# Optimization experiments

Measured on AMD Instinct MI355X. Metric: run time of the kernel, lower is better.

Reference implementation:

```python
import jax, jax.numpy as jnp
import numpy as np

B, L, N, T, D, V, C = 128, 512, 1023, 511, 256, 50000, 511
EPS = 1e-6


def circular_correlation(a, b):
    # c_k = sum_i a_i * b_{(i+k) mod d}  == irfft(conj(rfft(a)) * rfft(b))
    d = a.shape[-1]
    c = jnp.fft.irfft(jnp.conj(jnp.fft.rfft(a, axis=-1)) * jnp.fft.rfft(b, axis=-1), n=d, axis=-1)
    return c / (jnp.linalg.norm(c, axis=-1, keepdims=True) + EPS)


def setup_inputs() -> dict:
    key = jax.random.key(0)
    k1, k2, k3, k4, k5, k6, k7, k8 = jax.random.split(key, 8)
    num_node = jnp.full((B,), N, dtype=jnp.int64 if jax.config.jax_enable_x64 else jnp.int32)
    # leaf slot index: leaves occupy node slots 0..L-1 (deterministic, no scatter collisions)
    slot = jnp.broadcast_to(jnp.arange(L, dtype=jnp.int32)[None, :], (B, L))
    vocab_id = jax.random.randint(k1, (B, L), 0, V, dtype=jnp.int32)
    leaf_content_id = jnp.stack([slot, vocab_id], axis=-1)  # [B, L, 2]
    content_mask = (jax.random.uniform(k2, (B, L)) < 0.9).astype(jnp.int32)
    ctype = jax.random.randint(k3, (B, T), 0, 3, dtype=jnp.int32)          # 0 = no-op, 1, 2 children
    parent = jax.random.randint(k4, (B, T), L, N, dtype=jnp.int32)         # internal node slots
    lchild = jax.random.randint(k5, (B, T), 0, N, dtype=jnp.int32)
    rchild = jax.random.randint(k6, (B, T), 0, N, dtype=jnp.int32)
    composition_info = jnp.stack([ctype, parent, lchild, rchild], axis=-1)  # [B, T, 4]
    emb_weight = jax.random.normal(k7, (V, D), dtype=jnp.float32) * 0.1
    lin_weight = jax.random.normal(k8, (C, D), dtype=jnp.float32) * 0.05
    lin_bias = jnp.zeros((C,), dtype=jnp.float32)
    return {"num_node": num_node, "leaf_content_id": leaf_content_id,
            "content_mask": content_mask, "composition_info": composition_info,
            "emb_weight": emb_weight, "lin_weight": lin_weight, "lin_bias": lin_bias}


def embed_leaf_nodes(leaf_content_id, content_mask, emb_weight):
    leaf_vec = emb_weight[leaf_content_id[:, :, 1]]          # [B, L, D]
    node_idx = leaf_content_id[:, :, 0]                      # [B, L]
    mask = content_mask != 0
    safe_idx = jnp.where(mask, node_idx, N)                  # N is out-of-bounds -> dropped
    vec = jnp.zeros((B, N, D), dtype=leaf_vec.dtype)
    vec = vec.at[jnp.arange(B)[:, None], safe_idx].set(leaf_vec, mode="drop")
    norm = jnp.linalg.norm(vec, axis=2, keepdims=True) + EPS
    return vec / norm


def compose(vec, composition_info):
    bidx = jnp.arange(B)

    def step(v, info):  # info: [B, 4] for one tree level
        t, p, l, r = info[:, 0], info[:, 1], info[:, 2], info[:, 3]
        safe_p = jnp.where(t > 0, p, 0)
        lv = v[bidx, l]                                      # [B, D]
        rv = v[bidx, r]
        two = circular_correlation(lv, rv)
        cur = v[bidx, safe_p]
        val = jnp.where((t == 1)[:, None], lv,
                        jnp.where((t == 2)[:, None], two, cur))
        return v.at[bidx, safe_p].set(val), None

    vec, _ = jax.lax.scan(step, vec, jnp.swapaxes(composition_info, 0, 1))
    return vec


def reference(num_node, leaf_content_id, content_mask, composition_info,
              emb_weight, lin_weight, lin_bias):
    vec = embed_leaf_nodes(leaf_content_id, content_mask, emb_weight)
    vec = compose(vec, composition_info)
    out = jnp.einsum("bnd,cd->bnc", vec, lin_weight) + lin_bias
    return out
```

## Files before the change

kernel.cpp:

```cpp
#include <hip/hip_runtime.h>

#define NB 128
#define NL 512
#define NN 1023
#define NT 511
#define ND 256
#define NC 511
#define EPSF 1e-6f

#define SRC_ZERO (-1)
#define SLOTC 4096
#define STEPC 8192

typedef __attribute__((ext_vector_type(8))) short short8;
typedef __attribute__((ext_vector_type(4))) float f32x4;

__device__ __forceinline__ unsigned short f2bf(float f) {
  unsigned u = __builtin_bit_cast(unsigned, f);
  u += 0x7FFFu + ((u >> 16) & 1u);
  return (unsigned short)(u >> 16);
}

__global__ void __launch_bounds__(256) embed_scatter(
    const int* __restrict__ lcid, const int* __restrict__ cmask,
    const float* __restrict__ emb, float* __restrict__ leafbuf,
    unsigned short* __restrict__ vecb) {
  int rid  = blockIdx.x * 4 + (threadIdx.x >> 6);
  int lane = threadIdx.x & 63;
  int slot = lcid[2 * rid];
  int vid  = lcid[2 * rid + 1];
  int msk  = cmask[rid];
  int b    = rid >> 9;
  float4 v = {0.f, 0.f, 0.f, 0.f};
  if (msk) v = ((const float4*)(emb + (size_t)vid * ND))[lane];
  float ss = v.x * v.x + v.y * v.y + v.z * v.z + v.w * v.w;
#pragma unroll
  for (int off = 32; off > 0; off >>= 1) ss += __shfl_down(ss, off, 64);
  ss = __shfl(ss, 0, 64);
  float inv = 1.0f / (sqrtf(ss) + EPSF);
  float4 o;
  o.x = v.x * inv; o.y = v.y * inv; o.z = v.z * inv; o.w = v.w * inv;
  ((float4*)(leafbuf + ((size_t)b * 512 + slot) * ND))[lane] = o;
  uint2 pk;
  pk.x = (unsigned)f2bf(o.x) | ((unsigned)f2bf(o.y) << 16);
  pk.y = (unsigned)f2bf(o.z) | ((unsigned)f2bf(o.w) << 16);
  ((uint2*)(vecb + ((size_t)b * NN + slot) * ND))[lane] = pk;
}

__global__ void __launch_bounds__(1024) compose_kernel(
    const int* __restrict__ info, const int* __restrict__ lcid,
    const int* __restrict__ cmask, const float* __restrict__ leafbuf,
    float* __restrict__ outbuf, int* __restrict__ fsrcG) {
  const int b    = blockIdx.x;
  const int tid  = threadIdx.x;
  const int lane = tid & 63;
  const int wav  = tid >> 6;

  __shared__ int4 sinfo4[NT];
  __shared__ int lwl[NT], lwr[NT], fwr[NT];
  __shared__ int ptr_[NT];
  __shared__ int lsA[NT], rsA[NT];
  __shared__ int lvl[NT], fsrc[NT];
  __shared__ int schedS[NT], schedL[NT], schedR[NT];
  __shared__ int offs[512], cnt[512], cnt2[512];
  __shared__ unsigned char deadF[NT], liveF[NT], lzero[512];
  __shared__ float a_st[16][256], b_st[16][512];
  __shared__ int changed, smax;

  const float* lb = leafbuf + (size_t)b * 512 * ND;
  float*       ob = outbuf + (size_t)b * NT * ND;

  const int4* ib4 = (const int4*)(info + (size_t)b * NT * 4);
  for (int i = tid; i < NT; i += 1024) sinfo4[i] = ib4[i];
  if (tid < 512) lzero[tid] = 1;
  if (tid == 0) smax = 0;
  __syncthreads();
  if (tid < NL) {
    int row = lcid[((size_t)b * NL + tid) * 2];
    lzero[row] = (cmask[(size_t)b * NL + tid] == 0) ? 1 : 0;
  }
  __syncthreads();

  const int t = tid;
  int4 m1 = {0, 0, 0, 0};
  if (t < NT) m1 = sinfo4[t];
  int l1 = -1, r1 = -1, f1 = -1;
  const int prow = 512 + t;
  for (int tp = 0; tp < NT; ++tp) {
    int4 wi = sinfo4[tp];
    if (wi.x > 0) {
      if (t < NT && tp < t) { if (wi.y == m1.z) l1 = tp; if (wi.y == m1.w) r1 = tp; }
      if (wi.y == prow) f1 = tp;
    }
  }
  if (t < NT) { lwl[t] = l1; lwr[t] = r1; fwr[t] = f1; }
  __syncthreads();

  if (t < NT) {
    int v;
    if (m1.x == 2) v = SLOTC + t;
    else if (m1.x == 1) {
      if (m1.z < 512) v = m1.z;
      else v = (l1 >= 0) ? (STEPC + l1) : SRC_ZERO;
    } else v = SRC_ZERO;
    ptr_[t] = v;
  }
  __syncthreads();
  for (int it = 0; it < 10; ++it) {
    int v = 0;
    if (t < NT) { v = ptr_[t]; if (v >= STEPC) v = ptr_[v - STEPC]; }
    __syncthreads();
    if (t < NT) ptr_[t] = v;
    __syncthreads();
  }

  auto normv = [&](int v) -> int {
    if (v >= 0 && v < 512 && lzero[v]) return SRC_ZERO;
    return v;
  };
  auto collapseW = [&](int wstep) -> int {
    int v = (sinfo4[wstep].x == 2) ? (SLOTC + wstep) : ptr_[wstep];
    return normv(v);
  };
  if (t < NT) {
    if (m1.x == 2) {
      int a = (m1.z < 512) ? normv(m1.z) : ((l1 >= 0) ? collapseW(l1) : SRC_ZERO);
      int c = (m1.w < 512) ? normv(m1.w) : ((r1 >= 0) ? collapseW(r1) : SRC_ZERO);
      lsA[t] = a; rsA[t] = c;
      deadF[t] = (a == SRC_ZERO || c == SRC_ZERO) ? 1 : 0;
    } else {
      deadF[t] = 0;
    }
    liveF[t] = 0;
    fsrc[t] = (f1 >= 0) ? collapseW(f1) : SRC_ZERO;
  }
  __syncthreads();

  for (int rounds = 0; rounds < NT; ++rounds) {
    if (tid == 0) changed = 0;
    __syncthreads();
    if (t < NT && m1.x == 2 && !deadF[t]) {
      int a = lsA[t], c = rsA[t];
      if (a >= SLOTC && deadF[a - SLOTC]) { a = SRC_ZERO; lsA[t] = a; }
      if (c >= SLOTC && deadF[c - SLOTC]) { c = SRC_ZERO; rsA[t] = c; }
      if (a == SRC_ZERO || c == SRC_ZERO) { deadF[t] = 1; changed = 1; }
    }
    __syncthreads();
    if (!changed) break;
    __syncthreads();
  }

  if (t < NT) {
    int f = fsrc[t];
    if (f >= SLOTC && deadF[f - SLOTC]) { f = SRC_ZERO; fsrc[t] = f; }
    if (f >= SLOTC) liveF[f - SLOTC] = 1;
  }
  __syncthreads();
  for (int rounds = 0; rounds < NT; ++rounds) {
    if (tid == 0) changed = 0;
    __syncthreads();
    if (t < NT && m1.x == 2 && liveF[t] && !deadF[t]) {
      int a = lsA[t], c = rsA[t];
      if (a >= SLOTC && !liveF[a - SLOTC]) { liveF[a - SLOTC] = 1; changed = 1; }
      if (c >= SLOTC && !liveF[c - SLOTC]) { liveF[c - SLOTC] = 1; changed = 1; }
    }
    __syncthreads();
    if (!changed) break;
    __syncthreads();
  }

  const bool isLive = (t < NT && m1.x == 2 && liveF[t] && !deadF[t]);

  if (t < NT) lvl[t] = 0;
  __syncthreads();
  for (int rounds = 0; rounds < NT; ++rounds) {
    if (tid == 0) changed = 0;
    __syncthreads();
    if (isLive) {
      int nl = 1, a = lsA[t], c = rsA[t];
      if (a >= SLOTC) { int dl = lvl[a - SLOTC] + 1; if (dl > nl) nl = dl; }
      if (c >= SLOTC) { int dl = lvl[c - SLOTC] + 1; if (dl > nl) nl = dl; }
      if (nl > lvl[t]) { lvl[t] = nl; changed = 1; }
    }
    __syncthreads();
    if (!changed) break;
    __syncthreads();
  }
  if (isLive) atomicMax(&smax, lvl[t]);

  if (tid < 512) { cnt[tid] = 0; cnt2[tid] = 0; }
  __syncthreads();
  if (isLive) atomicAdd(&cnt[lvl[t]], 1);
  __syncthreads();
  if (tid < 512) offs[tid] = cnt[tid];
  __syncthreads();
  for (int k = 1; k < 512; k <<= 1) {
    int v = 0;
    if (tid < 512) { v = offs[tid]; if (tid >= k) v += offs[tid - k]; }
    __syncthreads();
    if (tid < 512) offs[tid] = v;
    __syncthreads();
  }
  if (isLive) {
    int d = lvl[t];
    int pos = offs[d - 1] + atomicAdd(&cnt2[d], 1);
    schedS[pos] = t; schedL[pos] = lsA[t]; schedR[pos] = rsA[t];
  }
  __syncthreads();

  const int maxd = smax;
  for (int d = 1; d <= maxd; ++d) {
    const int base = offs[d - 1];
    const int nops = cnt[d];
    const int nch  = (nops + 15) >> 4;
    for (int ch = 0; ch < nch; ++ch) {
      int rel = ch * 16 + wav;
      if (rel < nops) {
        int my = base + rel;
        int tt = schedS[my], ls = schedL[my], rs = schedR[my];
        const float* pa = (ls < 512) ? lb + (size_t)ls * ND
                                     : ob + (size_t)(ls - SLOTC) * ND;
        const float* pb = (rs < 512) ? lb + (size_t)rs * ND
                                     : ob + (size_t)(rs - SLOTC) * ND;
        float4 av = ((const float4*)pa)[lane];
        float4 bv = ((const float4*)pb)[lane];
        ((float4*)a_st[wav])[lane] = av;
        ((float4*)b_st[wav])[lane]      = bv;
        ((float4*)b_st[wav])[lane + 64] = bv;
        const float4* a4 = (const float4*)a_st[wav];
        const float4* b4 = (const float4*)b_st[wav];
        float c0 = 0.f, c1 = 0.f, c2 = 0.f, c3 = 0.f;
        float4 B0 = b4[lane];
#pragma unroll 8
        for (int i = 0; i < 64; ++i) {
          float4 A  = a4[i];
          float4 B1 = b4[lane + i + 1];
          c0 += A.x * B0.x + A.y * B0.y + A.z * B0.z + A.w * B0.w;
          c1 += A.x * B0.y + A.y * B0.z + A.z * B0.w + A.w * B1.x;
          c2 += A.x * B0.z + A.y * B0.w + A.z * B1.x + A.w * B1.y;
          c3 += A.x * B0.w + A.y * B1.x + A.z * B1.y + A.w * B1.z;
          B0 = B1;
        }
        float ss = c0 * c0 + c1 * c1 + c2 * c2 + c3 * c3;
#pragma unroll
        for (int off = 32; off > 0; off >>= 1) ss += __shfl_down(ss, off, 64);
        ss = __shfl(ss, 0, 64);
        float inv = 1.f / (sqrtf(ss) + EPSF);
        float4 res;
        res.x = c0 * inv; res.y = c1 * inv; res.z = c2 * inv; res.w = c3 * inv;
        ((float4*)(ob + (size_t)tt * ND))[lane] = res;
      }
    }
    __syncthreads();
  }

  for (int i = tid; i < NT; i += 1024) fsrcG[b * NT + i] = fsrc[i];
}

__global__ void __launch_bounds__(256) gather_rows(
    const int* __restrict__ fsrcG, const float* __restrict__ leafbuf,
    const float* __restrict__ outbuf, unsigned short* __restrict__ vecb) {
  int rid  = blockIdx.x * 4 + (threadIdx.x >> 6);
  int lane = threadIdx.x & 63;
  int b    = rid / NT;
  int idx  = rid - b * NT;
  int s    = fsrcG[rid];
  float4 v = {0.f, 0.f, 0.f, 0.f};
  if (s >= 0) {
    const float* src = (s < 512)
        ? (leafbuf + ((size_t)b * 512 + s) * ND)
        : (outbuf + ((size_t)b * NT + (s - SLOTC)) * ND);
    v = ((const float4*)src)[lane];
  }
  uint2 pk;
  pk.x = (unsigned)f2bf(v.x) | ((unsigned)f2bf(v.y) << 16);
  pk.y = (unsigned)f2bf(v.z) | ((unsigned)f2bf(v.w) << 16);
  ((uint2*)(vecb + ((size_t)b * NN + 512 + idx) * ND))[lane] = pk;
}

__global__ void __launch_bounds__(256) cvt_w(
    const float* __restrict__ src, unsigned short* __restrict__ o) {
  int i   = blockIdx.x * 256 + threadIdx.x;
  int row = (i * 8) >> 8;
  uint4 r = {0u, 0u, 0u, 0u};
  if (row < NC) {
    const float4* v4 = (const float4*)src;
    float4 x = v4[2 * i], y = v4[2 * i + 1];
    r.x = (unsigned)f2bf(x.x) | ((unsigned)f2bf(x.y) << 16);
    r.y = (unsigned)f2bf(x.z) | ((unsigned)f2bf(x.w) << 16);
    r.z = (unsigned)f2bf(y.x) | ((unsigned)f2bf(y.y) << 16);
    r.w = (unsigned)f2bf(y.z) | ((unsigned)f2bf(y.w) << 16);
  }
  ((uint4*)o)[i] = r;
}

__global__ void __launch_bounds__(256) gemm_kernel(
    const short* __restrict__ A, const short* __restrict__ W,
    const float* __restrict__ bias, float* __restrict__ out) {
  __shared__ short As[128 * 64];
  __shared__ short Ws[128 * 64];
  int tid  = threadIdx.x;
  int lane = tid & 63;
  int w    = tid >> 6;
  int c0   = blockIdx.x * 128;
  int m0   = blockIdx.y * 128;
  int wm   = (w & 1) * 64;
  int wc   = (w >> 1) * 64;
  int frow = lane & 15;
  int quad = lane >> 4;
  f32x4 acc[4][4];
#pragma unroll
  for (int i = 0; i < 4; ++i)
#pragma unroll
    for (int j = 0; j < 4; ++j) acc[i][j] = (f32x4){0.f, 0.f, 0.f, 0.f};

  for (int k0 = 0; k0 < ND; k0 += 64) {
#pragma unroll
    for (int i = 0; i < 4; ++i) {
      int idx = i * 256 + tid;
      int row = idx >> 3;
      int ch  = idx & 7;
      const short* ga = A + (size_t)(m0 + row) * ND + k0 + ch * 8;
      const short* gw = W + (size_t)(c0 + row) * ND + k0 + ch * 8;
      __builtin_amdgcn_global_load_lds(
          (const __attribute__((address_space(1))) void*)ga,
          (__attribute__((address_space(3))) void*)(As + idx * 8), 16, 0, 0);
      __builtin_amdgcn_global_load_lds(
          (const __attribute__((address_space(1))) void*)gw,
          (__attribute__((address_space(3))) void*)(Ws + idx * 8), 16, 0, 0);
    }
    __syncthreads();
#pragma unroll
    for (int ks = 0; ks < 2; ++ks) {
      short8 af[4], wf[4];
#pragma unroll
      for (int mi = 0; mi < 4; ++mi)
        af[mi] = *(const short8*)(As + (wm + mi * 16 + frow) * 64 + ks * 32 + quad * 8);
#pragma unroll
      for (int ci = 0; ci < 4; ++ci)
        wf[ci] = *(const short8*)(Ws + (wc + ci * 16 + frow) * 64 + ks * 32 + quad * 8);
#pragma unroll
      for (int mi = 0; mi < 4; ++mi)
#pragma unroll
        for (int ci = 0; ci < 4; ++ci)
          acc[mi][ci] = __builtin_amdgcn_mfma_f32_16x16x32_bf16(
              af[mi], wf[ci], acc[mi][ci], 0, 0, 0);
    }
    __syncthreads();
  }
#pragma unroll
  for (int mi = 0; mi < 4; ++mi) {
#pragma unroll
    for (int ci = 0; ci < 4; ++ci) {
      int col = c0 + wc + ci * 16 + frow;
      if (col < NC) {
        float bv = bias[col];
#pragma unroll
        for (int r = 0; r < 4; ++r) {
          int m = m0 + wm + mi * 16 + quad * 4 + r;
          out[(size_t)m * NC + col] = acc[mi][ci][r] + bv;
        }
      }
    }
  }
}

extern "C" void kernel_launch(void* const* d_in, const int* in_sizes, int n_in,
                              void* d_out, int out_size, void* d_ws, size_t ws_size,
                              hipStream_t stream) {
  const int*   lcid  = (const int*)d_in[1];
  const int*   cmask = (const int*)d_in[2];
  const int*   cinfo = (const int*)d_in[3];
  const float* emb   = (const float*)d_in[4];
  const float* lw    = (const float*)d_in[5];
  const float* lb    = (const float*)d_in[6];
  float*       out   = (float*)d_out;

  char* ws = (char*)d_ws;
  float*          leafbuf = (float*)ws;
  float*          outbuf  = (float*)(ws + 67108864);
  unsigned short* vecb    = (unsigned short*)(ws + 134086656);
  unsigned short* wb      = (unsigned short*)(ws + 201129984);
  int*            fsrcG   = (int*)d_out;

  embed_scatter<<<NB * NL / 4, 256, 0, stream>>>(lcid, cmask, emb, leafbuf, vecb);
  cvt_w<<<(512 * ND / 8) / 256, 256, 0, stream>>>(lw, wb);
  compose_kernel<<<NB, 1024, 0, stream>>>(cinfo, lcid, cmask, leafbuf, outbuf, fsrcG);
  gather_rows<<<NB * NT / 4, 256, 0, stream>>>(fsrcG, leafbuf, outbuf, vecb);
  gemm_kernel<<<dim3(4, 1023), 256, 0, stream>>>(
      (const short*)vecb, (const short*)wb, lb, out);
}
```

Before: 557.2 us.

## Split compose into prep/exec kernels and overlap leaf GEMM with tree execution

The single compose kernel becomes two. A prep kernel resolves the schedule, and it also absorbs leaf embedding and weight conversion. An exec kernel runs tree evaluation for each batch plus the internal-row gather. In that same exec launch, extra blocks compute the leaf-row GEMM so it overlaps with the serial tree work, and a separate GEMM handles the internal rows afterwards. The schedule is staged through the output buffer's internal-row region, and the correlation inner loop uses packed float2 FMAs. This removes launches and idle CUs during the latency-bound compose, at the cost of more complex shared-memory unions and ordering dependencies through d_out.

Measured after the change: 680.3 us. 22.1% more time.

```diff
diff --git a/kernel.cpp b/kernel.cpp
--- a/kernel.cpp
+++ b/kernel.cpp
@@ -12,8 +12,16 @@
 #define SLOTC 4096
 #define STEPC 8192
 
+#define OFF_MAXD 0
+#define OFF_OFFS 8
+#define OFF_S 524
+#define OFF_L 1036
+#define OFF_R 1548
+#define OFF_F 2060
+
 typedef __attribute__((ext_vector_type(8))) short short8;
 typedef __attribute__((ext_vector_type(4))) float f32x4;
+typedef __attribute__((ext_vector_type(2))) float f32x2;
 
 __device__ __forceinline__ unsigned short f2bf(float f) {
   unsigned u = __builtin_bit_cast(unsigned, f);
@@ -21,79 +29,93 @@
   return (unsigned short)(u >> 16);
 }
 
-__global__ void __launch_bounds__(256) embed_scatter(
-    const int* __restrict__ lcid, const int* __restrict__ cmask,
-    const float* __restrict__ emb, float* __restrict__ leafbuf,
-    unsigned short* __restrict__ vecb) {
-  int rid  = blockIdx.x * 4 + (threadIdx.x >> 6);
-  int lane = threadIdx.x & 63;
-  int slot = lcid[2 * rid];
-  int vid  = lcid[2 * rid + 1];
-  int msk  = cmask[rid];
-  int b    = rid >> 9;
-  float4 v = {0.f, 0.f, 0.f, 0.f};
-  if (msk) v = ((const float4*)(emb + (size_t)vid * ND))[lane];
-  float ss = v.x * v.x + v.y * v.y + v.z * v.z + v.w * v.w;
-#pragma unroll
-  for (int off = 32; off > 0; off >>= 1) ss += __shfl_down(ss, off, 64);
-  ss = __shfl(ss, 0, 64);
-  float inv = 1.0f / (sqrtf(ss) + EPSF);
-  float4 o;
-  o.x = v.x * inv; o.y = v.y * inv; o.z = v.z * inv; o.w = v.w * inv;
-  ((float4*)(leafbuf + ((size_t)b * 512 + slot) * ND))[lane] = o;
-  uint2 pk;
-  pk.x = (unsigned)f2bf(o.x) | ((unsigned)f2bf(o.y) << 16);
-  pk.y = (unsigned)f2bf(o.z) | ((unsigned)f2bf(o.w) << 16);
-  ((uint2*)(vecb + ((size_t)b * NN + slot) * ND))[lane] = pk;
-}
-
-__global__ void __launch_bounds__(1024) compose_kernel(
+struct ResolveSh {
+  int4 sinfo4[NT];
+  int lwl[NT], lwr[NT], fwr[NT];
+  int ptr_[NT];
+  int lsA[NT], rsA[NT];
+  int lvl[NT], fsrc[NT];
+  int schedS[NT], schedL[NT], schedR[NT];
+  int offs[512], cnt[512], cnt2[512];
+  unsigned char deadF[NT], liveF[NT], lzero[512];
+  int changed, smax;
+};
+
+__global__ void __launch_bounds__(512) prep_kernel(
     const int* __restrict__ info, const int* __restrict__ lcid,
-    const int* __restrict__ cmask, const float* __restrict__ leafbuf,
-    float* __restrict__ outbuf, int* __restrict__ fsrcG) {
-  const int b    = blockIdx.x;
-  const int tid  = threadIdx.x;
-  const int lane = tid & 63;
-  const int wav  = tid >> 6;
-
-  __shared__ int4 sinfo4[NT];
-  __shared__ int lwl[NT], lwr[NT], fwr[NT];
-  __shared__ int ptr_[NT];
-  __shared__ int lsA[NT], rsA[NT];
-  __shared__ int lvl[NT], fsrc[NT];
-  __shared__ int schedS[NT], schedL[NT], schedR[NT];
-  __shared__ int offs[512], cnt[512], cnt2[512];
-  __shared__ unsigned char deadF[NT], liveF[NT], lzero[512];
-  __shared__ float a_st[16][256], b_st[16][512];
-  __shared__ int changed, smax;
-
-  const float* lb = leafbuf + (size_t)b * 512 * ND;
-  float*       ob = outbuf + (size_t)b * NT * ND;
-
+    const int* __restrict__ cmask, const float* __restrict__ emb,
+    const float* __restrict__ lw, float* __restrict__ leafbuf,
+    unsigned short* __restrict__ vecb, unsigned short* __restrict__ wb,
+    int* __restrict__ schedO) {
+  __shared__ ResolveSh sh;
+  const int bid = blockIdx.x;
+  const int tid = threadIdx.x;
+
+  if (bid >= 8320) {
+    int i   = (bid - 8320) * 512 + tid;
+    int row = i >> 5;
+    uint4 r = {0u, 0u, 0u, 0u};
+    if (row < NC) {
+      const float4* v4 = (const float4*)lw;
+      float4 x = v4[2 * i], y = v4[2 * i + 1];
+      r.x = (unsigned)f2bf(x.x) | ((unsigned)f2bf(x.y) << 16);
+      r.y = (unsigned)f2bf(x.z) | ((unsigned)f2bf(x.w) << 16);
+      r.z = (unsigned)f2bf(y.x) | ((unsigned)f2bf(y.y) << 16);
+      r.w = (unsigned)f2bf(y.z) | ((unsigned)f2bf(y.w) << 16);
+    }
+    ((uint4*)wb)[i] = r;
+    return;
+  }
+
+  if (bid >= 128) {
+    int rid  = (bid - 128) * 8 + (tid >> 6);
+    int lane = tid & 63;
+    int slot = lcid[2 * rid];
+    int vid  = lcid[2 * rid + 1];
+    int msk  = cmask[rid];
+    int b    = rid >> 9;
+    float4 v = {0.f, 0.f, 0.f, 0.f};
+    if (msk) v = ((const float4*)(emb + (size_t)vid * ND))[lane];
+    float ss = v.x * v.x + v.y * v.y + v.z * v.z + v.w * v.w;
+#pragma unroll
+    for (int off = 32; off > 0; off >>= 1) ss += __shfl_down(ss, off, 64);
+    ss = __shfl(ss, 0, 64);
+    float inv = 1.0f / (sqrtf(ss) + EPSF);
+    float4 o;
+    o.x = v.x * inv; o.y = v.y * inv; o.z = v.z * inv; o.w = v.w * inv;
+    ((float4*)(leafbuf + ((size_t)b * 512 + slot) * ND))[lane] = o;
+    uint2 pk;
+    pk.x = (unsigned)f2bf(o.x) | ((unsigned)f2bf(o.y) << 16);
+    pk.y = (unsigned)f2bf(o.z) | ((unsigned)f2bf(o.w) << 16);
+    ((uint2*)(vecb + ((size_t)b * NN + slot) * ND))[lane] = pk;
+    return;
+  }
+
+  const int b = bid;
   const int4* ib4 = (const int4*)(info + (size_t)b * NT * 4);
-  for (int i = tid; i < NT; i += 1024) sinfo4[i] = ib4[i];
-  if (tid < 512) lzero[tid] = 1;
-  if (tid == 0) smax = 0;
+  for (int i = tid; i < NT; i += 512) sh.sinfo4[i] = ib4[i];
+  if (tid < 512) sh.lzero[tid] = 1;
+  if (tid == 0) sh.smax = 0;
   __syncthreads();
   if (tid < NL) {
     int row = lcid[((size_t)b * NL + tid) * 2];
-    lzero[row] = (cmask[(size_t)b * NL + tid] == 0) ? 1 : 0;
+    sh.lzero[row] = (cmask[(size_t)b * NL + tid] == 0) ? 1 : 0;
   }
   __syncthreads();
 
   const int t = tid;
   int4 m1 = {0, 0, 0, 0};
-  if (t < NT) m1 = sinfo4[t];
+  if (t < NT) m1 = sh.sinfo4[t];
   int l1 = -1, r1 = -1, f1 = -1;
   const int prow = 512 + t;
   for (int tp = 0; tp < NT; ++tp) {
-    int4 wi = sinfo4[tp];
+    int4 wi = sh.sinfo4[tp];
     if (wi.x > 0) {
       if (t < NT && tp < t) { if (wi.y == m1.z) l1 = tp; if (wi.y == m1.w) r1 = tp; }
       if (wi.y == prow) f1 = tp;
     }
   }
-  if (t < NT) { lwl[t] = l1; lwr[t] = r1; fwr[t] = f1; }
+  if (t < NT) { sh.lwl[t] = l1; sh.lwr[t] = r1; sh.fwr[t] = f1; }
   __syncthreads();
 
   if (t < NT) {
@@ -103,198 +125,300 @@
       if (m1.z < 512) v = m1.z;
       else v = (l1 >= 0) ? (STEPC + l1) : SRC_ZERO;
     } else v = SRC_ZERO;
-    ptr_[t] = v;
+    sh.ptr_[t] = v;
   }
   __syncthreads();
   for (int it = 0; it < 10; ++it) {
     int v = 0;
-    if (t < NT) { v = ptr_[t]; if (v >= STEPC) v = ptr_[v - STEPC]; }
-    __syncthreads();
-    if (t < NT) ptr_[t] = v;
+    if (t < NT) { v = sh.ptr_[t]; if (v >= STEPC) v = sh.ptr_[v - STEPC]; }
+    __syncthreads();
+    if (t < NT) sh.ptr_[t] = v;
     __syncthreads();
   }
 
   auto normv = [&](int v) -> int {
-    if (v >= 0 && v < 512 && lzero[v]) return SRC_ZERO;
+    if (v >= 0 && v < 512 && sh.lzero[v]) return SRC_ZERO;
     return v;
   };
   auto collapseW = [&](int wstep) -> int {
-    int v = (sinfo4[wstep].x == 2) ? (SLOTC + wstep) : ptr_[wstep];
+    int v = (sh.sinfo4[wstep].x == 2) ? (SLOTC + wstep) : sh.ptr_[wstep];
     return normv(v);
   };
   if (t < NT) {
     if (m1.x == 2) {
       int a = (m1.z < 512) ? normv(m1.z) : ((l1 >= 0) ? collapseW(l1) : SRC_ZERO);
       int c = (m1.w < 512) ? normv(m1.w) : ((r1 >= 0) ? collapseW(r1) : SRC_ZERO);
-      lsA[t] = a; rsA[t] = c;
-      deadF[t] = (a == SRC_ZERO || c == SRC_ZERO) ? 1 : 0;
+      sh.lsA[t] = a; sh.rsA[t] = c;
+      sh.deadF[t] = (a == SRC_ZERO || c == SRC_ZERO) ? 1 : 0;
     } else {
-      deadF[t] = 0;
-    }
-    liveF[t] = 0;
-    fsrc[t] = (f1 >= 0) ? collapseW(f1) : SRC_ZERO;
+      sh.deadF[t] = 0;
+    }
+    sh.liveF[t] = 0;
+    sh.fsrc[t] = (f1 >= 0) ? collapseW(f1) : SRC_ZERO;
   }
   __syncthreads();
 
   for (int rounds = 0; rounds < NT; ++rounds) {
-    if (tid == 0) changed = 0;
-    __syncthreads();
-    if (t < NT && m1.x == 2 && !deadF[t]) {
-      int a = lsA[t], c = rsA[t];
-      if (a >= SLOTC && deadF[a - SLOTC]) { a = SRC_ZERO; lsA[t] = a; }
-      if (c >= SLOTC && deadF[c - SLOTC]) { c = SRC_ZERO; rsA[t] = c; }
-      if (a == SRC_ZERO || c == SRC_ZERO) { deadF[t] = 1; changed = 1; }
-    }
-    __syncthreads();
-    if (!changed) break;
+    if (tid == 0) sh.changed = 0;
+    __syncthreads();
+    if (t < NT && m1.x == 2 && !sh.deadF[t]) {
+      int a = sh.lsA[t], c = sh.rsA[t];
+      if (a >= SLOTC && sh.deadF[a - SLOTC]) { a = SRC_ZERO; sh.lsA[t] = a; }
+      if (c >= SLOTC && sh.deadF[c - SLOTC]) { c = SRC_ZERO; sh.rsA[t] = c; }
+      if (a == SRC_ZERO || c == SRC_ZERO) { sh.deadF[t] = 1; sh.changed = 1; }
+    }
+    __syncthreads();
+    if (!sh.changed) break;
     __syncthreads();
   }
 
   if (t < NT) {
-    int f = fsrc[t];
-    if (f >= SLOTC && deadF[f - SLOTC]) { f = SRC_ZERO; fsrc[t] = f; }
-    if (f >= SLOTC) liveF[f - SLOTC] = 1;
+    int f = sh.fsrc[t];
+    if (f >= SLOTC && sh.deadF[f - SLOTC]) { f = SRC_ZERO; sh.fsrc[t] = f; }
+    if (f >= SLOTC) sh.liveF[f - SLOTC] = 1;
   }
   __syncthreads();
   for (int rounds = 0; rounds < NT; ++rounds) {
-    if (tid == 0) changed = 0;
-    __syncthreads();
-    if (t < NT && m1.x == 2 && liveF[t] && !deadF[t]) {
-      int a = lsA[t], c = rsA[t];
-      if (a >= SLOTC && !liveF[a - SLOTC]) { liveF[a - SLOTC] = 1; changed = 1; }
-      if (c >= SLOTC && !liveF[c - SLOTC]) { liveF[c - SLOTC] = 1; changed = 1; }
-    }
-    __syncthreads();
-    if (!changed) break;
-    __syncthreads();
-  }
-
-  const bool isLive = (t < NT && m1.x == 2 && liveF[t] && !deadF[t]);
-
-  if (t < NT) lvl[t] = 0;
+    if (tid == 0) sh.changed = 0;
+    __syncthreads();
+    if (t < NT && m1.x == 2 && sh.liveF[t] && !sh.deadF[t]) {
+      int a = sh.lsA[t], c = sh.rsA[t];
+      if (a >= SLOTC && !sh.liveF[a - SLOTC]) { sh.liveF[a - SLOTC] = 1; sh.changed = 1; }
+      if (c >= SLOTC && !sh.liveF[c - SLOTC]) { sh.liveF[c - SLOTC] = 1; sh.changed = 1; }
+    }
+    __syncthreads();
+    if (!sh.changed) break;
+    __syncthreads();
+  }
+
+  const bool isLive = (t < NT && m1.x == 2 && sh.liveF[t] && !sh.deadF[t]);
+
+  if (t < NT) sh.lvl[t] = 0;
   __syncthreads();
   for (int rounds = 0; rounds < NT; ++rounds) {
-    if (tid == 0) changed = 0;
+    if (tid == 0) sh.changed = 0;
     __syncthreads();
     if (isLive) {
-      int nl = 1, a = lsA[t], c = rsA[t];
-      if (a >= SLOTC) { int dl = lvl[a - SLOTC] + 1; if (dl > nl) nl = dl; }
-      if (c >= SLOTC) { int dl = lvl[c - SLOTC] + 1; if (dl > nl) nl = dl; }
-      if (nl > lvl[t]) { lvl[t] = nl; changed = 1; }
-    }
-    __syncthreads();
-    if (!changed) break;
-    __syncthreads();
-  }
-  if (isLive) atomicMax(&smax, lvl[t]);
-
-  if (tid < 512) { cnt[tid] = 0; cnt2[tid] = 0; }
-  __syncthreads();
-  if (isLive) atomicAdd(&cnt[lvl[t]], 1);
-  __syncthreads();
-  if (tid < 512) offs[tid] = cnt[tid];
+      int nl = 1, a = sh.lsA[t], c = sh.rsA[t];
+      if (a >= SLOTC) { int dl = sh.lvl[a - SLOTC] + 1; if (dl > nl) nl = dl; }
+      if (c >= SLOTC) { int dl = sh.lvl[c - SLOTC] + 1; if (dl > nl) nl = dl; }
+      if (nl > sh.lvl[t]) { sh.lvl[t] = nl; sh.changed = 1; }
+    }
+    __syncthreads();
+    if (!sh.changed) break;
+    __syncthreads();
+  }
+  if (isLive) atomicMax(&sh.smax, sh.lvl[t]);
+
+  if (tid < 512) { sh.cnt[tid] = 0; sh.cnt2[tid] = 0; }
+  __syncthreads();
+  if (isLive) atomicAdd(&sh.cnt[sh.lvl[t]], 1);
+  __syncthreads();
+  if (tid < 512) sh.offs[tid] = sh.cnt[tid];
   __syncthreads();
   for (int k = 1; k < 512; k <<= 1) {
     int v = 0;
-    if (tid < 512) { v = offs[tid]; if (tid >= k) v += offs[tid - k]; }
-    __syncthreads();
-    if (tid < 512) offs[tid] = v;
+    if (tid < 512) { v = sh.offs[tid]; if (tid >= k) v += sh.offs[tid - k]; }
+    __syncthreads();
+    if (tid < 512) sh.offs[tid] = v;
     __syncthreads();
   }
   if (isLive) {
-    int d = lvl[t];
-    int pos = offs[d - 1] + atomicAdd(&cnt2[d], 1);
-    schedS[pos] = t; schedL[pos] = lsA[t]; schedR[pos] = rsA[t];
-  }
-  __syncthreads();
-
-  const int maxd = smax;
-  for (int d = 1; d <= maxd; ++d) {
-    const int base = offs[d - 1];
-    const int nops = cnt[d];
-    const int nch  = (nops + 15) >> 4;
-    for (int ch = 0; ch < nch; ++ch) {
-      int rel = ch * 16 + wav;
-      if (rel < nops) {
-        int my = base + rel;
-        int tt = schedS[my], ls = schedL[my], rs = schedR[my];
-        const float* pa = (ls < 512) ? lb + (size_t)ls * ND
-                                     : ob + (size_t)(ls - SLOTC) * ND;
-        const float* pb = (rs < 512) ? lb + (size_t)rs * ND
-                                     : ob + (size_t)(rs - SLOTC) * ND;
-        float4 av = ((const float4*)pa)[lane];
-        float4 bv = ((const float4*)pb)[lane];
-        ((float4*)a_st[wav])[lane] = av;
-        ((float4*)b_st[wav])[lane]      = bv;
-        ((float4*)b_st[wav])[lane + 64] = bv;
-        const float4* a4 = (const float4*)a_st[wav];
-        const float4* b4 = (const float4*)b_st[wav];
-        float c0 = 0.f, c1 = 0.f, c2 = 0.f, c3 = 0.f;
-        float4 B0 = b4[lane];
+    int d = sh.lvl[t];
+    int pos = sh.offs[d - 1] + atomicAdd(&sh.cnt2[d], 1);
+    sh.schedS[pos] = t; sh.schedL[pos] = sh.lsA[t]; sh.schedR[pos] = sh.rsA[t];
+  }
+  __syncthreads();
+
+  int* g = schedO + ((size_t)b * NN + 512) * NC;
+  for (int i = tid; i < NT; i += 512) {
+    g[OFF_S + i] = sh.schedS[i];
+    g[OFF_L + i] = sh.schedL[i];
+    g[OFF_R + i] = sh.schedR[i];
+    g[OFF_F + i] = sh.fsrc[i];
+  }
+  g[OFF_OFFS + tid] = sh.offs[tid];
+  if (tid == 0) g[OFF_MAXD] = sh.smax;
+}
+
+struct ExecSh {
+  int schedS[NT], schedL[NT], schedR[NT];
+  int offs[512];
+  int fsrc[NT];
+  int maxd;
+  float a_st[16][256];
+  float b_st[16][512];
+};
+struct GemmSh {
+  short As[256 * 64];
+  short Ws[128 * 64];
+};
+union Sh2 { ExecSh e; GemmSh g; };
+
+__global__ void __launch_bounds__(1024) exec_kernel(
+    const float* __restrict__ leafbuf, float* __restrict__ outbuf,
+    unsigned short* __restrict__ vecb, const short* __restrict__ wbs,
+    const float* __restrict__ bias, float* __restrict__ out,
+    const int* __restrict__ schedI) {
+  __shared__ Sh2 sh;
+  const int tid  = threadIdx.x;
+  const int lane = tid & 63;
+  const int wav  = tid >> 6;
+
+  if (blockIdx.x < NB) {
+    const int b = blockIdx.x;
+    const float* lb = leafbuf + (size_t)b * 512 * ND;
+    float*       ob = outbuf + (size_t)b * NT * ND;
+    const int*   g  = schedI + ((size_t)b * NN + 512) * NC;
+    for (int i = tid; i < NT; i += 1024) {
+      sh.e.schedS[i] = g[OFF_S + i];
+      sh.e.schedL[i] = g[OFF_L + i];
+      sh.e.schedR[i] = g[OFF_R + i];
+      sh.e.fsrc[i]   = g[OFF_F + i];
+    }
+    if (tid < 512) sh.e.offs[tid] = g[OFF_OFFS + tid];
+    if (tid == 0) sh.e.maxd = g[OFF_MAXD];
+    __syncthreads();
+    const int maxd = sh.e.maxd;
+
+    for (int d = 1; d <= maxd; ++d) {
+      const int base = sh.e.offs[d - 1];
+      const int nops = sh.e.offs[d] - base;
+      const int nch  = (nops + 15) >> 4;
+      for (int ch = 0; ch < nch; ++ch) {
+        int rel = ch * 16 + wav;
+        if (rel < nops) {
+          int my = base + rel;
+          int tt = sh.e.schedS[my], ls = sh.e.schedL[my], rs = sh.e.schedR[my];
+          const float* pa = (ls < 512) ? lb + (size_t)ls * ND
+                                       : ob + (size_t)(ls - SLOTC) * ND;
+          const float* pb = (rs < 512) ? lb + (size_t)rs * ND
+                                       : ob + (size_t)(rs - SLOTC) * ND;
+          float4 av = ((const float4*)pa)[lane];
+          float4 bv = ((const float4*)pb)[lane];
+          ((float4*)sh.e.a_st[wav])[lane]      = av;
+          ((float4*)sh.e.b_st[wav])[lane]      = bv;
+          ((float4*)sh.e.b_st[wav])[lane + 64] = bv;
+          const float4* a4 = (const float4*)sh.e.a_st[wav];
+          const float4* b4 = (const float4*)sh.e.b_st[wav];
+          f32x2 p01 = {0.f, 0.f}, p23 = {0.f, 0.f};
+          float4 B0 = b4[lane];
 #pragma unroll 8
-        for (int i = 0; i < 64; ++i) {
-          float4 A  = a4[i];
-          float4 B1 = b4[lane + i + 1];
-          c0 += A.x * B0.x + A.y * B0.y + A.z * B0.z + A.w * B0.w;
-          c1 += A.x * B0.y + A.y * B0.z + A.z * B0.w + A.w * B1.x;
-          c2 += A.x * B0.z + A.y * B0.w + A.z * B1.x + A.w * B1.y;
-          c3 += A.x * B0.w + A.y * B1.x + A.z * B1.y + A.w * B1.z;
-          B0 = B1;
+          for (int i = 0; i < 64; ++i) {
+            float4 A  = a4[i];
+            float4 B1 = b4[lane + i + 1];
+            f32x2 ax = {A.x, A.x}, ay = {A.y, A.y}, az = {A.z, A.z}, aw = {A.w, A.w};
+            f32x2 b01  = {B0.x, B0.y}, b23  = {B0.z, B0.w};
+            f32x2 b12  = {B0.y, B0.z}, b3n0 = {B0.w, B1.x};
+            f32x2 bn01 = {B1.x, B1.y}, bn12 = {B1.y, B1.z};
+            p01 += ax * b01;  p23 += ax * b23;
+            p01 += ay * b12;  p23 += ay * b3n0;
+            p01 += az * b23;  p23 += az * bn01;
+            p01 += aw * b3n0; p23 += aw * bn12;
+            B0 = B1;
+          }
+          float c0 = p01.x, c1 = p01.y, c2 = p23.x, c3 = p23.y;
+          float ss = c0 * c0 + c1 * c1 + c2 * c2 + c3 * c3;
+#pragma unroll
+          for (int off = 32; off > 0; off >>= 1) ss += __shfl_down(ss, off, 64);
+          ss = __shfl(ss, 0, 64);
+          float inv = 1.f / (sqrtf(ss) + EPSF);
+          float4 res;
+          res.x = c0 * inv; res.y = c1 * inv; res.z = c2 * inv; res.w = c3 * inv;
+          ((float4*)(ob + (size_t)tt * ND))[lane] = res;
         }
-        float ss = c0 * c0 + c1 * c1 + c2 * c2 + c3 * c3;
-#pragma unroll
-        for (int off = 32; off > 0; off >>= 1) ss += __shfl_down(ss, off, 64);
-        ss = __shfl(ss, 0, 64);
-        float inv = 1.f / (sqrtf(ss) + EPSF);
-        float4 res;
-        res.x = c0 * inv; res.y = c1 * inv; res.z = c2 * inv; res.w = c3 * inv;
-        ((float4*)(ob + (size_t)tt * ND))[lane] = res;
       }
-    }
-    __syncthreads();
-  }
-
-  for (int i = tid; i < NT; i += 1024) fsrcG[b * NT + i] = fsrc[i];
+      __syncthreads();
+    }
+
+    for (int i = wav; i < NT; i += 16) {
+      int s = sh.e.fsrc[i];
+      float4 v = {0.f, 0.f, 0.f, 0.f};
+      if (s >= 0) {
+        const float* src = (s < 512) ? lb + (size_t)s * ND
+                                     : ob + (size_t)(s - SLOTC) * ND;
+        v = ((const float4*)src)[lane];
+      }
+      uint2 pk;
+      pk.x = (unsigned)f2bf(v.x) | ((unsigned)f2bf(v.y) << 16);
+      pk.y = (unsigned)f2bf(v.z) | ((unsigned)f2bf(v.w) << 16);
+      ((uint2*)(vecb + ((size_t)b * NN + 512 + i) * ND))[lane] = pk;
+    }
+    return;
+  }
+
+  const int gidx = blockIdx.x - NB;
+  const int b  = gidx >> 3;
+  const int mt = (gidx >> 2) & 1;
+  const int ct = gidx & 3;
+  const short* A = (const short*)vecb + ((size_t)b * NN + mt * 256) * ND;
+  const int c0   = ct * 128;
+  const int wr   = wav >> 1;
+  const int wc   = wav & 1;
+  const int frow = lane & 15;
+  const int quad = lane >> 4;
+  f32x4 acc[2][4];
+#pragma unroll
+  for (int i = 0; i < 2; ++i)
+#pragma unroll
+    for (int j = 0; j < 4; ++j) acc[i][j] = (f32x4){0.f, 0.f, 0.f, 0.f};
+
+  for (int k0 = 0; k0 < ND; k0 += 64) {
+#pragma unroll
+    for (int i = 0; i < 2; ++i) {
+      int idx = i * 1024 + tid;
+      int row = idx >> 3;
+      int chn = idx & 7;
+      const short* ga = A + (size_t)row * ND + k0 + chn * 8;
+      __builtin_amdgcn_global_load_lds(
+          (const __attribute__((address_space(1))) void*)ga,
+          (__attribute__((address_space(3))) void*)(sh.g.As + idx * 8), 16, 0, 0);
+    }
+    {
+      int row = tid >> 3;
+      int chn = tid & 7;
+      const short* gw = wbs + (size_t)(c0 + row) * ND + k0 + chn * 8;
+      __builtin_amdgcn_global_load_lds(
+          (const __attribute__((address_space(1))) void*)gw,
+          (__attribute__((address_space(3))) void*)(sh.g.Ws + tid * 8), 16, 0, 0);
+    }
+    __syncthreads();
+#pragma unroll
+    for (int ks = 0; ks < 2; ++ks) {
+      short8 af[2], wf[4];
+#pragma unroll
+      for (int mi = 0; mi < 2; ++mi)
+        af[mi] = *(const short8*)(sh.g.As + (wr * 32 + mi * 16 + frow) * 64 + ks * 32 + quad * 8);
+#pragma unroll
+      for (int ci = 0; ci < 4; ++ci)
+        wf[ci] = *(const short8*)(sh.g.Ws + (wc * 64 + ci * 16 + frow) * 64 + ks * 32 + quad * 8);
+#pragma unroll
+      for (int mi = 0; mi < 2; ++mi)
+#pragma unroll
+        for (int ci = 0; ci < 4; ++ci)
+          acc[mi][ci] = __builtin_amdgcn_mfma_f32_16x16x32_bf16(
+              af[mi], wf[ci], acc[mi][ci], 0, 0, 0);
+    }
+    __syncthreads();
+  }
+#pragma unroll
+  for (int mi = 0; mi < 2; ++mi) {
+#pragma unroll
+    for (int ci = 0; ci < 4; ++ci) {
+      int col = c0 + wc * 64 + ci * 16 + frow;
+      if (col < NC) {
+        float bv = bias[col];
+#pragma unroll
+        for (int r = 0; r < 4; ++r) {
+          int n = mt * 256 + wr * 32 + mi * 16 + quad * 4 + r;
+          out[((size_t)b * NN + n) * NC + col] = acc[mi][ci][r] + bv;
+        }
+      }
+    }
+  }
 }
 
-__global__ void __launch_bounds__(256) gather_rows(
-    const int* __restrict__ fsrcG, const float* __restrict__ leafbuf,
-    const float* __restrict__ outbuf, unsigned short* __restrict__ vecb) {
-  int rid  = blockIdx.x * 4 + (threadIdx.x >> 6);
-  int lane = threadIdx.x & 63;
-  int b    = rid / NT;
-  int idx  = rid - b * NT;
-  int s    = fsrcG[rid];
-  float4 v = {0.f, 0.f, 0.f, 0.f};
-  if (s >= 0) {
-    const float* src = (s < 512)
-        ? (leafbuf + ((size_t)b * 512 + s) * ND)
-        : (outbuf + ((size_t)b * NT + (s - SLOTC)) * ND);
-    v = ((const float4*)src)[lane];
-  }
-  uint2 pk;
-  pk.x = (unsigned)f2bf(v.x) | ((unsigned)f2bf(v.y) << 16);
-  pk.y = (unsigned)f2bf(v.z) | ((unsigned)f2bf(v.w) << 16);
-  ((uint2*)(vecb + ((size_t)b * NN + 512 + idx) * ND))[lane] = pk;
-}
-
-__global__ void __launch_bounds__(256) cvt_w(
-    const float* __restrict__ src, unsigned short* __restrict__ o) {
-  int i   = blockIdx.x * 256 + threadIdx.x;
-  int row = (i * 8) >> 8;
-  uint4 r = {0u, 0u, 0u, 0u};
-  if (row < NC) {
-    const float4* v4 = (const float4*)src;
-    float4 x = v4[2 * i], y = v4[2 * i + 1];
-    r.x = (unsigned)f2bf(x.x) | ((unsigned)f2bf(x.y) << 16);
-    r.y = (unsigned)f2bf(x.z) | ((unsigned)f2bf(x.w) << 16);
-    r.z = (unsigned)f2bf(y.x) | ((unsigned)f2bf(y.y) << 16);
-    r.w = (unsigned)f2bf(y.z) | ((unsigned)f2bf(y.w) << 16);
-  }
-  ((uint4*)o)[i] = r;
-}
-
-__global__ void __launch_bounds__(256) gemm_kernel(
+__global__ void __launch_bounds__(256) gemm_internal(
     const short* __restrict__ A, const short* __restrict__ W,
     const float* __restrict__ bias, float* __restrict__ out) {
   __shared__ short As[128 * 64];
@@ -303,7 +427,9 @@
   int lane = tid & 63;
   int w    = tid >> 6;
   int c0   = blockIdx.x * 128;
-  int m0   = blockIdx.y * 128;
+  int b    = blockIdx.y >> 2;
+  int mt   = blockIdx.y & 3;
+  size_t mbase = (size_t)b * NN + 512 + mt * 128;
   int wm   = (w & 1) * 64;
   int wc   = (w >> 1) * 64;
   int frow = lane & 15;
@@ -319,9 +445,9 @@
     for (int i = 0; i < 4; ++i) {
       int idx = i * 256 + tid;
       int row = idx >> 3;
-      int ch  = idx & 7;
-      const short* ga = A + (size_t)(m0 + row) * ND + k0 + ch * 8;
-      const short* gw = W + (size_t)(c0 + row) * ND + k0 + ch * 8;
+      int chn = idx & 7;
+      const short* ga = A + (mbase + row) * ND + k0 + chn * 8;
+      const short* gw = W + (size_t)(c0 + row) * ND + k0 + chn * 8;
       __builtin_amdgcn_global_load_lds(
           (const __attribute__((address_space(1))) void*)ga,
           (__attribute__((address_space(3))) void*)(As + idx * 8), 16, 0, 0);
@@ -357,8 +483,9 @@
         float bv = bias[col];
 #pragma unroll
         for (int r = 0; r < 4; ++r) {
-          int m = m0 + wm + mi * 16 + quad * 4 + r;
-          out[(size_t)m * NC + col] = acc[mi][ci][r] + bv;
+          int n = 512 + mt * 128 + wm + mi * 16 + quad * 4 + r;
+          if (n < NN)
+            out[((size_t)b * NN + n) * NC + col] = acc[mi][ci][r] + bv;
         }
       }
     }
@@ -373,7 +500,7 @@
   const int*   cinfo = (const int*)d_in[3];
   const float* emb   = (const float*)d_in[4];
   const float* lw    = (const float*)d_in[5];
-  const float* lb    = (const float*)d_in[6];
+  const float* lbias = (const float*)d_in[6];
   float*       out   = (float*)d_out;
 
   char* ws = (char*)d_ws;
@@ -381,12 +508,12 @@
   float*          outbuf  = (float*)(ws + 67108864);
   unsigned short* vecb    = (unsigned short*)(ws + 134086656);
   unsigned short* wb      = (unsigned short*)(ws + 201129984);
-  int*            fsrcG   = (int*)d_out;
-
-  embed_scatter<<<NB * NL / 4, 256, 0, stream>>>(lcid, cmask, emb, leafbuf, vecb);
-  cvt_w<<<(512 * ND / 8) / 256, 256, 0, stream>>>(lw, wb);
-  compose_kernel<<<NB, 1024, 0, stream>>>(cinfo, lcid, cmask, leafbuf, outbuf, fsrcG);
-  gather_rows<<<NB * NT / 4, 256, 0, stream>>>(fsrcG, leafbuf, outbuf, vecb);
-  gemm_kernel<<<dim3(4, 1023), 256, 0, stream>>>(
-      (const short*)vecb, (const short*)wb, lb, out);
+
+  prep_kernel<<<8352, 512, 0, stream>>>(cinfo, lcid, cmask, emb, lw,
+                                        leafbuf, vecb, wb, (int*)d_out);
+  exec_kernel<<<1152, 1024, 0, stream>>>(leafbuf, outbuf, vecb,
+                                         (const short*)wb, lbias, out,
+                                         (const int*)d_out);
+  gemm_internal<<<dim3(4, 512), 256, 0, stream>>>(
+      (const short*)vecb, (const short*)wb, lbias, out);
 }
```

## Swizzle GEMM LDS tiles, stage epilogue through LDS, fuse weight conversion

Applied to the files above, without the earlier changes.

XOR-swizzles the 16-byte chunk index when loading A and W tiles into LDS, and applies the same swizzle on the MFMA fragment reads, to remove LDS bank conflicts. The GEMM epilogue now writes accumulators into an LDS staging buffer that reuses the tile memory, so each lane stores whole contiguous rows of output for coalesced writes. The separate bf16 weight-conversion kernel is folded into extra blocks of the embed kernel to save one launch. The staging buffer's reuse of tile memory is not guarded by a barrier against other waves; since each wave uses its own slice and the loop ends with a sync, this is likely safe.

New measurement: 559.5 us. About the same (+0.4%).

```diff
diff --git a/kernel.cpp b/kernel.cpp
--- a/kernel.cpp
+++ b/kernel.cpp
@@ -23,8 +23,24 @@
 
 __global__ void __launch_bounds__(256) embed_scatter(
     const int* __restrict__ lcid, const int* __restrict__ cmask,
-    const float* __restrict__ emb, float* __restrict__ leafbuf,
-    unsigned short* __restrict__ vecb) {
+    const float* __restrict__ emb, const float* __restrict__ lw,
+    float* __restrict__ leafbuf, unsigned short* __restrict__ vecb,
+    unsigned short* __restrict__ wb) {
+  if (blockIdx.x >= 16384) {
+    int i   = (blockIdx.x - 16384) * 256 + threadIdx.x;
+    int row = i >> 5;
+    uint4 r = {0u, 0u, 0u, 0u};
+    if (row < NC) {
+      const float4* v4 = (const float4*)lw;
+      float4 x = v4[2 * i], y = v4[2 * i + 1];
+      r.x = (unsigned)f2bf(x.x) | ((unsigned)f2bf(x.y) << 16);
+      r.y = (unsigned)f2bf(x.z) | ((unsigned)f2bf(x.w) << 16);
+      r.z = (unsigned)f2bf(y.x) | ((unsigned)f2bf(y.y) << 16);
+      r.w = (unsigned)f2bf(y.z) | ((unsigned)f2bf(y.w) << 16);
+    }
+    ((uint4*)wb)[i] = r;
+    return;
+  }
   int rid  = blockIdx.x * 4 + (threadIdx.x >> 6);
   int lane = threadIdx.x & 63;
   int slot = lcid[2 * rid];
@@ -278,27 +294,15 @@
   ((uint2*)(vecb + ((size_t)b * NN + 512 + idx) * ND))[lane] = pk;
 }
 
-__global__ void __launch_bounds__(256) cvt_w(
-    const float* __restrict__ src, unsigned short* __restrict__ o) {
-  int i   = blockIdx.x * 256 + threadIdx.x;
-  int row = (i * 8) >> 8;
-  uint4 r = {0u, 0u, 0u, 0u};
-  if (row < NC) {
-    const float4* v4 = (const float4*)src;
-    float4 x = v4[2 * i], y = v4[2 * i + 1];
-    r.x = (unsigned)f2bf(x.x) | ((unsigned)f2bf(x.y) << 16);
-    r.y = (unsigned)f2bf(x.z) | ((unsigned)f2bf(x.w) << 16);
-    r.z = (unsigned)f2bf(y.x) | ((unsigned)f2bf(y.y) << 16);
-    r.w = (unsigned)f2bf(y.z) | ((unsigned)f2bf(y.w) << 16);
-  }
-  ((uint4*)o)[i] = r;
-}
+union GemmSh {
+  struct { short As[128 * 64]; short Ws[128 * 64]; } s;
+  float epi[4][16][65];
+};
 
 __global__ void __launch_bounds__(256) gemm_kernel(
     const short* __restrict__ A, const short* __restrict__ W,
     const float* __restrict__ bias, float* __restrict__ out) {
-  __shared__ short As[128 * 64];
-  __shared__ short Ws[128 * 64];
+  __shared__ GemmSh sh;
   int tid  = threadIdx.x;
   int lane = tid & 63;
   int w    = tid >> 6;
@@ -320,25 +324,32 @@
       int idx = i * 256 + tid;
       int row = idx >> 3;
       int ch  = idx & 7;
-      const short* ga = A + (size_t)(m0 + row) * ND + k0 + ch * 8;
-      const short* gw = W + (size_t)(c0 + row) * ND + k0 + ch * 8;
+      int chs = ch ^ (row & 7);
+      const short* ga = A + (size_t)(m0 + row) * ND + k0 + chs * 8;
+      const short* gw = W + (size_t)(c0 + row) * ND + k0 + chs * 8;
       __builtin_amdgcn_global_load_lds(
           (const __attribute__((address_space(1))) void*)ga,
-          (__attribute__((address_space(3))) void*)(As + idx * 8), 16, 0, 0);
+          (__attribute__((address_space(3))) void*)(sh.s.As + idx * 8), 16, 0, 0);
       __builtin_amdgcn_global_load_lds(
           (const __attribute__((address_space(1))) void*)gw,
-          (__attribute__((address_space(3))) void*)(Ws + idx * 8), 16, 0, 0);
+          (__attribute__((address_space(3))) void*)(sh.s.Ws + idx * 8), 16, 0, 0);
     }
     __syncthreads();
 #pragma unroll
     for (int ks = 0; ks < 2; ++ks) {
       short8 af[4], wf[4];
 #pragma unroll
-      for (int mi = 0; mi < 4; ++mi)
-        af[mi] = *(const short8*)(As + (wm + mi * 16 + frow) * 64 + ks * 32 + quad * 8);
-#pragma unroll
-      for (int ci = 0; ci < 4; ++ci)
-        wf[ci] = *(const short8*)(Ws + (wc + ci * 16 + frow) * 64 + ks * 32 + quad * 8);
+      for (int mi = 0; mi < 4; ++mi) {
+        int r = wm + mi * 16 + frow;
+        int cc = (ks * 4 + quad) ^ (r & 7);
+        af[mi] = *(const short8*)(sh.s.As + r * 64 + cc * 8);
+      }
+#pragma unroll
+      for (int ci = 0; ci < 4; ++ci) {
+        int r = wc + ci * 16 + frow;
+        int cc = (ks * 4 + quad) ^ (r & 7);
+        wf[ci] = *(const short8*)(sh.s.Ws + r * 64 + cc * 8);
+      }
 #pragma unroll
       for (int mi = 0; mi < 4; ++mi)
 #pragma unroll
@@ -348,19 +359,21 @@
     }
     __syncthreads();
   }
+
+  int colg = c0 + wc + lane;
+  float bv = (colg < NC) ? bias[colg] : 0.f;
 #pragma unroll
   for (int mi = 0; mi < 4; ++mi) {
 #pragma unroll
-    for (int ci = 0; ci < 4; ++ci) {
-      int col = c0 + wc + ci * 16 + frow;
-      if (col < NC) {
-        float bv = bias[col];
-#pragma unroll
-        for (int r = 0; r < 4; ++r) {
-          int m = m0 + wm + mi * 16 + quad * 4 + r;
-          out[(size_t)m * NC + col] = acc[mi][ci][r] + bv;
-        }
-      }
+    for (int ci = 0; ci < 4; ++ci)
+#pragma unroll
+      for (int r = 0; r < 4; ++r)
+        sh.epi[w][quad * 4 + r][ci * 16 + frow] = acc[mi][ci][r];
+    if (colg < NC) {
+      int mrow = m0 + wm + mi * 16;
+#pragma unroll
+      for (int rr = 0; rr < 16; ++rr)
+        out[(size_t)(mrow + rr) * NC + colg] = sh.epi[w][rr][lane] + bv;
     }
   }
 }
@@ -373,7 +386,7 @@
   const int*   cinfo = (const int*)d_in[3];
   const float* emb   = (const float*)d_in[4];
   const float* lw    = (const float*)d_in[5];
-  const float* lb    = (const float*)d_in[6];
+  const float* lbias = (const float*)d_in[6];
   float*       out   = (float*)d_out;
 
   char* ws = (char*)d_ws;
@@ -383,10 +396,11 @@
   unsigned short* wb      = (unsigned short*)(ws + 201129984);
   int*            fsrcG   = (int*)d_out;
 
-  embed_scatter<<<NB * NL / 4, 256, 0, stream>>>(lcid, cmask, emb, leafbuf, vecb);
-  cvt_w<<<(512 * ND / 8) / 256, 256, 0, stream>>>(lw, wb);
-  compose_kernel<<<NB, 1024, 0, stream>>>(cinfo, lcid, cmask, leafbuf, outbuf, fsrcG);
+  embed_scatter<<<16448, 256, 0, stream>>>(lcid, cmask, emb, lw,
+                                           leafbuf, vecb, wb);
+  compose_kernel<<<NB, 1024, 0, stream>>>(cinfo, lcid, cmask, leafbuf,
+                                          outbuf, fsrcG);
   gather_rows<<<NB * NT / 4, 256, 0, stream>>>(fsrcG, leafbuf, outbuf, vecb);
   gemm_kernel<<<dim3(4, 1023), 256, 0, stream>>>(
-      (const short*)vecb, (const short*)wb, lb, out);
-}
+      (const short*)vecb, (const short*)wb, lbias, out);
+}
```
